# Kernel optimization log

Hardware: AMD Instinct MI355X
Metric: run time of the kernel (lower is better)

The kernel has to match this reference:

```python
import jax, jax.numpy as jnp
import numpy as np

NUM_GRAPHS = 128

def _gcn_conv(x, W, b, src, dst, deg_inv_sqrt, n_nodes):
    # PyG GCNConv: h = X W; out[dst] += d^-1/2[src] * d^-1/2[dst] * h[src]; out += b
    h = x @ W
    norm = deg_inv_sqrt[src] * deg_inv_sqrt[dst]  # [E]
    msg = h[src] * norm[:, None]                  # [E, C]
    out = jax.ops.segment_sum(msg, dst, num_segments=n_nodes)
    return out + b


def setup_inputs() -> dict:
    key = jax.random.key(0)
    k1, k2, k3, k4, k5 = jax.random.split(key, 5)
    n_nodes, n_edges, c_in, c_hid = 50000, 800000, 256, 256
    x = jax.random.normal(k1, (n_nodes, c_in), dtype=jnp.float32)
    edge_index = jax.random.randint(k2, (2, n_edges), 0, n_nodes, dtype=jnp.int64)
    batch = jnp.sort(jax.random.randint(k3, (n_nodes,), 0, NUM_GRAPHS, dtype=jnp.int64))
    s1 = 1.0 / np.sqrt(c_in)
    s2 = 1.0 / np.sqrt(c_hid)
    W1 = jax.random.uniform(k4, (c_in, c_hid), jnp.float32, -s1, s1)
    b1 = jnp.zeros((c_hid,), jnp.float32)
    W2 = jax.random.uniform(k5, (c_hid, c_hid), jnp.float32, -s2, s2)
    b2 = jnp.zeros((c_hid,), jnp.float32)
    return {"x": x, "edge_index": edge_index, "batch": batch,
            "W1": W1, "b1": b1, "W2": W2, "b2": b2}


def reference(x, edge_index, batch, W1, b1, W2, b2):
    n_nodes = x.shape[0]
    # add self-loops (GCNConv default add_self_loops=True)
    loops = jnp.arange(n_nodes, dtype=edge_index.dtype)
    src = jnp.concatenate([edge_index[0], loops])
    dst = jnp.concatenate([edge_index[1], loops])
    deg = jax.ops.segment_sum(jnp.ones_like(dst, dtype=x.dtype), dst, num_segments=n_nodes)
    deg_inv_sqrt = jnp.where(deg > 0, jax.lax.rsqrt(deg), 0.0)

    h = jax.nn.relu(_gcn_conv(x, W1, b1, src, dst, deg_inv_sqrt, n_nodes))
    # dropout p=0.2 is identity in eval mode
    h = jax.nn.relu(_gcn_conv(h, W2, b2, src, dst, deg_inv_sqrt, n_nodes))

    # global mean pool over graph ids
    sums = jax.ops.segment_sum(h, batch, num_segments=NUM_GRAPHS)
    cnts = jax.ops.segment_sum(jnp.ones((n_nodes,), h.dtype), batch, num_segments=NUM_GRAPHS)
    return sums / jnp.maximum(cnts, 1.0)[:, None]
```

## Files before the change

kernel.cpp:

```cpp
#include <hip/hip_runtime.h>

#define NCH 256
#define NS  16

typedef short short8 __attribute__((ext_vector_type(8)));
typedef float f32x4  __attribute__((ext_vector_type(4)));

__device__ __forceinline__ float b2f(unsigned short u) {
    union { unsigned int i; float f; } x; x.i = ((unsigned int)u) << 16; return x.f;
}
__device__ __forceinline__ unsigned short f2b(float f) {
    unsigned int u = __float_as_uint(f);
    unsigned int r = (u + 0x7FFFu + ((u >> 16) & 1u)) >> 16;
    return (unsigned short)r;
}

#define GLOAD_LDS16(gptr, lptr) \
    __builtin_amdgcn_global_load_lds((const __attribute__((address_space(1))) void*)(gptr), \
                                     (__attribute__((address_space(3))) void*)(lptr), 16, 0, 0)

__global__ __launch_bounds__(256) void k_init_deg(int* __restrict__ deg, int n) {
    int i = blockIdx.x * 256 + threadIdx.x;
    if (i < n) deg[i] = 1;
}

__global__ __launch_bounds__(256) void k_hist(const int* __restrict__ dst, int E,
                                              int* __restrict__ deg) {
    int e = blockIdx.x * 256 + threadIdx.x;
    if (e < E) atomicAdd(&deg[dst[e]], 1);
}

__global__ __launch_bounds__(256) void k_scan_blk(const int* __restrict__ deg,
                                                  int* __restrict__ part,
                                                  int* __restrict__ bsum, int N) {
    __shared__ int sm[256];
    int t = threadIdx.x;
    int base = blockIdx.x * 1024 + t * 4;
    int v[4]; int s = 0;
#pragma unroll
    for (int j = 0; j < 4; ++j) {
        int i = base + j;
        int d = (i < N) ? (deg[i] - 1) : 0;
        v[j] = d; s += d;
    }
    sm[t] = s; __syncthreads();
#pragma unroll
    for (int off = 1; off < 256; off <<= 1) {
        int u = (t >= off) ? sm[t - off] : 0;
        __syncthreads();
        sm[t] += u;
        __syncthreads();
    }
    int excl = sm[t] - s;
#pragma unroll
    for (int j = 0; j < 4; ++j) {
        int i = base + j;
        if (i < N) part[i] = excl;
        excl += v[j];
    }
    if (t == 255) bsum[blockIdx.x] = sm[255];
}

__global__ void k_scan_top(int* __restrict__ bsum, int nb, int* __restrict__ rowptr_end) {
    int t = threadIdx.x;
    int orig = (t < nb) ? bsum[t] : 0;
    int v = orig;
#pragma unroll
    for (int off = 1; off < 64; off <<= 1) {
        int u = __shfl_up(v, off, 64);
        if (t >= off) v += u;
    }
    if (t < nb) bsum[t] = v - orig;
    if (t == 63) *rowptr_end = v;
}

__global__ __launch_bounds__(256) void k_finalize(const int* __restrict__ deg,
                                                  int* __restrict__ row_ptr,
                                                  const int* __restrict__ boff,
                                                  int* __restrict__ cursor,
                                                  float* __restrict__ dinv, int N) {
    int i = blockIdx.x * 256 + threadIdx.x;
    if (i < N) {
        int rp = row_ptr[i] + boff[i >> 10];
        row_ptr[i] = rp;
        cursor[i]  = rp;
        dinv[i] = rsqrtf((float)deg[i]);
    }
}

__global__ __launch_bounds__(256) void k_scatter(const int* __restrict__ src,
                                                 const int* __restrict__ dst, int E,
                                                 int* __restrict__ cursor,
                                                 int* __restrict__ col) {
    int e = blockIdx.x * 256 + threadIdx.x;
    if (e < E) {
        int d = dst[e];
        int pos = atomicAdd(&cursor[d], 1);
        col[pos] = src[e];
    }
}

__global__ __launch_bounds__(256) void k_cast8(const float* __restrict__ in,
                                               unsigned short* __restrict__ out, int n8) {
    int i = blockIdx.x * 256 + threadIdx.x;
    if (i < n8) {
        const float4* p = (const float4*)(in + (size_t)i * 8);
        float4 a = p[0], b = p[1];
        unsigned short us[8];
        us[0] = f2b(a.x); us[1] = f2b(a.y); us[2] = f2b(a.z); us[3] = f2b(a.w);
        us[4] = f2b(b.x); us[5] = f2b(b.y); us[6] = f2b(b.z); us[7] = f2b(b.w);
        *(int4*)(out + (size_t)i * 8) = *(const int4*)us;
    }
}

__global__ __launch_bounds__(256) void k_castT(const float* __restrict__ W1,
                                               const float* __restrict__ W2,
                                               unsigned short* __restrict__ Wt1,
                                               unsigned short* __restrict__ Wt2) {
    int k = blockIdx.x, n = threadIdx.x;
    const float* W = blockIdx.y ? W2 : W1;
    unsigned short* Wt = blockIdx.y ? Wt2 : Wt1;
    Wt[(size_t)n * 256 + k] = f2b(W[(size_t)k * 256 + n]);
}

__global__ __launch_bounds__(256) void k_gemm_bf16(const unsigned short* __restrict__ A,
                                                   const unsigned short* __restrict__ Bt,
                                                   unsigned short* __restrict__ C, int M) {
    __shared__ unsigned short As[128 * 32];
    __shared__ unsigned short Bs[128 * 32];

    const int tid  = threadIdx.x;
    const int wid  = tid >> 6;
    const int lane = tid & 63;
    const int m0 = blockIdx.x * 128;
    const int n0 = blockIdx.y * 128;
    const int wr = wid >> 1, wc = wid & 1;

    const int srow = tid >> 2;
    const int skc  = (((tid & 3) ^ (srow & 3)) << 3);
    int arow0 = m0 + srow;       if (arow0 >= M) arow0 = M - 1;
    int arow1 = m0 + srow + 64;  if (arow1 >= M) arow1 = M - 1;
    const int brow0 = n0 + srow;
    const int brow1 = n0 + srow + 64;

    const unsigned short* gA0 = A  + (size_t)arow0 * NCH + skc;
    const unsigned short* gA1 = A  + (size_t)arow1 * NCH + skc;
    const unsigned short* gB0 = Bt + (size_t)brow0 * NCH + skc;
    const unsigned short* gB1 = Bt + (size_t)brow1 * NCH + skc;

    unsigned short* ldsA0 = As + (wid << 9);
    unsigned short* ldsA1 = As + 2048 + (wid << 9);
    unsigned short* ldsB0 = Bs + (wid << 9);
    unsigned short* ldsB1 = Bs + 2048 + (wid << 9);

    f32x4 acc[4][4];
#pragma unroll
    for (int i = 0; i < 4; ++i)
#pragma unroll
        for (int j = 0; j < 4; ++j) acc[i][j] = (f32x4){0.f, 0.f, 0.f, 0.f};

    const int lr = lane & 15;
    const int kcu = lane >> 4;

    for (int k0 = 0; k0 < 256; k0 += 32) {
        __syncthreads();
        GLOAD_LDS16(gA0 + k0, ldsA0);
        GLOAD_LDS16(gA1 + k0, ldsA1);
        GLOAD_LDS16(gB0 + k0, ldsB0);
        GLOAD_LDS16(gB1 + k0, ldsB1);
        __syncthreads();

        short8 af[4], bfr[4];
#pragma unroll
        for (int mf = 0; mf < 4; ++mf) {
            int row = wr * 64 + mf * 16 + lr;
            int lk = ((kcu ^ (row & 3)) << 3);
            af[mf] = *(const short8*)&As[row * 32 + lk];
        }
#pragma unroll
        for (int nf = 0; nf < 4; ++nf) {
            int row = wc * 64 + nf * 16 + lr;
            int lk = ((kcu ^ (row & 3)) << 3);
            bfr[nf] = *(const short8*)&Bs[row * 32 + lk];
        }
#pragma unroll
        for (int mf = 0; mf < 4; ++mf)
#pragma unroll
            for (int nf = 0; nf < 4; ++nf)
                acc[mf][nf] = __builtin_amdgcn_mfma_f32_16x16x32_bf16(af[mf], bfr[nf],
                                                                      acc[mf][nf], 0, 0, 0);
    }

#pragma unroll
    for (int mf = 0; mf < 4; ++mf) {
#pragma unroll
        for (int nf = 0; nf < 4; ++nf) {
            int rb = m0 + wr * 64 + mf * 16 + ((lane >> 4) << 2);
            int cc = n0 + wc * 64 + nf * 16 + lr;
#pragma unroll
            for (int r = 0; r < 4; ++r) {
                int row = rb + r;
                if (row < M) C[(size_t)row * NCH + cc] = f2b(acc[mf][nf][r]);
            }
        }
    }
}

__global__ __launch_bounds__(256) void k_agg_w(const unsigned short* __restrict__ h,
                                               const float* __restrict__ dinv,
                                               const int* __restrict__ row_ptr,
                                               const int* __restrict__ col,
                                               const float* __restrict__ bias,
                                               unsigned short* __restrict__ out, int M) {
    int v = blockIdx.x * 4 + (threadIdx.x >> 6);
    if (v >= M) return;
    const int lane = threadIdx.x & 63;
    const int half = lane >> 5;
    const int cb   = (lane & 31) << 3;

    float acc[8] = {};
    float dv = dinv[v];

    if (half == 0) {
        short8 hv = *(const short8*)&h[(size_t)v * NCH + cb];
#pragma unroll
        for (int i = 0; i < 8; ++i) acc[i] += dv * b2f((unsigned short)hv[i]);
    }

    int beg = row_ptr[v], end = row_ptr[v + 1];
    for (int idx = beg + half; idx < end; idx += 2) {
        int s = col[idx];
        float ws = dinv[s];
        short8 hs = *(const short8*)&h[(size_t)s * NCH + cb];
#pragma unroll
        for (int i = 0; i < 8; ++i) acc[i] += ws * b2f((unsigned short)hs[i]);
    }

#pragma unroll
    for (int i = 0; i < 8; ++i) acc[i] += __shfl_xor(acc[i], 32, 64);

    if (half == 0) {
        f32x4 bl = *(const f32x4*)&bias[cb];
        f32x4 bh = *(const f32x4*)&bias[cb + 4];
        unsigned short us[8];
#pragma unroll
        for (int i = 0; i < 8; ++i) {
            float b = (i < 4) ? bl[i] : bh[i - 4];
            us[i] = f2b(fmaxf(dv * acc[i] + b, 0.0f));
        }
        *(int4*)&out[(size_t)v * NCH + cb] = *(const int4*)us;
    }
}

__device__ __forceinline__ int lower_bound_i(const int* a, int n, int key) {
    int lo = 0, hi = n;
    while (lo < hi) {
        int mid = (lo + hi) >> 1;
        if (a[mid] < key) lo = mid + 1; else hi = mid;
    }
    return lo;
}

__global__ __launch_bounds__(64) void k_pool_a(const unsigned short* __restrict__ a,
                                               const int* __restrict__ batch,
                                               float* __restrict__ partial, int N) {
    int g = blockIdx.x, s = blockIdx.y;
    const int lane = threadIdx.x;
    const int half = lane >> 5;
    const int cb   = (lane & 31) << 3;

    int lo = lower_bound_i(batch, N, g);
    int hi = lower_bound_i(batch, N, g + 1);
    int cnt = hi - lo;
    int len = (cnt + NS - 1) / NS;
    int rlo = lo + s * len;
    int rhi = min(rlo + len, hi);

    float acc[8] = {};
    for (int r = rlo + half; r < rhi; r += 2) {
        short8 hv = *(const short8*)&a[(size_t)r * NCH + cb];
#pragma unroll
        for (int i = 0; i < 8; ++i) acc[i] += b2f((unsigned short)hv[i]);
    }
#pragma unroll
    for (int i = 0; i < 8; ++i) acc[i] += __shfl_xor(acc[i], 32, 64);

    if (half == 0) {
        float* p = partial + ((size_t)g * NS + s) * NCH + cb;
        *(f32x4*)p       = (f32x4){acc[0], acc[1], acc[2], acc[3]};
        *(f32x4*)(p + 4) = (f32x4){acc[4], acc[5], acc[6], acc[7]};
    }
}

__global__ __launch_bounds__(256) void k_pool_b(const float* __restrict__ partial,
                                                const int* __restrict__ batch,
                                                float* __restrict__ out, int N) {
    int g = blockIdx.x, ch = threadIdx.x;
    int lo = lower_bound_i(batch, N, g);
    int hi = lower_bound_i(batch, N, g + 1);
    float s = 0.0f;
#pragma unroll
    for (int k = 0; k < NS; ++k)
        s += partial[((size_t)g * NS + k) * NCH + ch];
    out[(size_t)g * NCH + ch] = s / (float)max(hi - lo, 1);
}

extern "C" void kernel_launch(void* const* d_in, const int* in_sizes, int n_in,
                              void* d_out, int out_size, void* d_ws, size_t ws_size,
                              hipStream_t stream) {
    const float* x     = (const float*)d_in[0];
    const int*   ei    = (const int*)d_in[1];
    const int*   batch = (const int*)d_in[2];
    const float* W1    = (const float*)d_in[3];
    const float* b1    = (const float*)d_in[4];
    const float* W2    = (const float*)d_in[5];
    const float* b2    = (const float*)d_in[6];
    float* out = (float*)d_out;

    const int M = in_sizes[0] / NCH;
    const int E = in_sizes[1] / 2;
    const int* src = ei;
    const int* dst = ei + E;

    char* w = (char*)d_ws;
    auto alloc = [&](size_t bytes) -> void* {
        void* p = (void*)w;
        w += (bytes + 255) & ~(size_t)255;
        return p;
    };
    int*   deg     = (int*)alloc((size_t)M * 4);
    float* dinv    = (float*)alloc((size_t)M * 4);
    int*   row_ptr = (int*)alloc((size_t)(M + 1) * 4);
    int*   cursor  = (int*)alloc((size_t)M * 4);
    int*   bsum    = (int*)alloc(64 * 4);
    int*   col     = (int*)alloc((size_t)E * 4);
    unsigned short* xb   = (unsigned short*)alloc((size_t)M * NCH * 2);
    unsigned short* bufP = (unsigned short*)alloc((size_t)M * NCH * 2);
    unsigned short* bufQ = (unsigned short*)alloc((size_t)M * NCH * 2);
    unsigned short* Wt1  = (unsigned short*)alloc((size_t)NCH * NCH * 2);
    unsigned short* Wt2  = (unsigned short*)alloc((size_t)NCH * NCH * 2);
    float* partial = (float*)alloc((size_t)128 * NS * NCH * 4);

    const int nb = (M + 1023) / 1024;

    k_cast8<<<(M * NCH / 8 + 255) / 256, 256, 0, stream>>>(x, xb, M * NCH / 8);
    k_castT<<<dim3(256, 2), 256, 0, stream>>>(W1, W2, Wt1, Wt2);

    k_init_deg<<<(M + 255) / 256, 256, 0, stream>>>(deg, M);
    k_hist<<<(E + 255) / 256, 256, 0, stream>>>(dst, E, deg);
    k_scan_blk<<<nb, 256, 0, stream>>>(deg, row_ptr, bsum, M);
    k_scan_top<<<1, 64, 0, stream>>>(bsum, nb, row_ptr + M);
    k_finalize<<<(M + 255) / 256, 256, 0, stream>>>(deg, row_ptr, bsum, cursor, dinv, M);
    k_scatter<<<(E + 255) / 256, 256, 0, stream>>>(src, dst, E, cursor, col);

    dim3 ggrid((M + 127) / 128, NCH / 128);

    k_gemm_bf16<<<ggrid, 256, 0, stream>>>(xb, Wt1, bufP, M);
    k_agg_w<<<(M + 3) / 4, 256, 0, stream>>>(bufP, dinv, row_ptr, col, b1, bufQ, M);
    k_gemm_bf16<<<ggrid, 256, 0, stream>>>(bufQ, Wt2, bufP, M);
    k_agg_w<<<(M + 3) / 4, 256, 0, stream>>>(bufP, dinv, row_ptr, col, b2, bufQ, M);
    k_pool_a<<<dim3(128, NS), 64, 0, stream>>>(bufQ, batch, partial, M);
    k_pool_b<<<128, 256, 0, stream>>>(partial, batch, out, M);
}
```

Measured before the change: 303.3 us.

## Use register-resident weight GEMM and prefetch packed edge weights in aggregation

Replaces the LDS-tiled GEMM with a persistent kernel in which each wave keeps its 64-column slice of the bf16 weight matrix in registers. Each block streams 16-row A tiles straight from global memory, double-buffering the next tile in registers. A new pre-pass packs each edge's source index and dinv[src] into an int2 array, so aggregation does one load per edge instead of two dependent ones. The aggregation loop is software-pipelined to keep two edges per half-wave in flight. The costs are high register pressure in the GEMM, no LDS sharing of A, an extra E-sized buffer, and one more kernel launch.

```diff
diff --git a/kernel.cpp b/kernel.cpp
--- a/kernel.cpp
+++ b/kernel.cpp
@@ -14,10 +14,6 @@
     unsigned int r = (u + 0x7FFFu + ((u >> 16) & 1u)) >> 16;
     return (unsigned short)r;
 }
-
-#define GLOAD_LDS16(gptr, lptr) \
-    __builtin_amdgcn_global_load_lds((const __attribute__((address_space(1))) void*)(gptr), \
-                                     (__attribute__((address_space(3))) void*)(lptr), 16, 0, 0)
 
 __global__ __launch_bounds__(256) void k_init_deg(int* __restrict__ deg, int n) {
     int i = blockIdx.x * 256 + threadIdx.x;
@@ -100,6 +96,16 @@
     }
 }
 
+__global__ __launch_bounds__(256) void k_wprep(const int* __restrict__ col,
+                                               const float* __restrict__ dinv,
+                                               int2* __restrict__ cw, int E) {
+    int i = blockIdx.x * 256 + threadIdx.x;
+    if (i < E) {
+        int s = col[i];
+        cw[i] = make_int2(s, __float_as_int(dinv[s]));
+    }
+}
+
 __global__ __launch_bounds__(256) void k_cast8(const float* __restrict__ in,
                                                unsigned short* __restrict__ out, int n8) {
     int i = blockIdx.x * 256 + threadIdx.x;
@@ -123,93 +129,73 @@
     Wt[(size_t)n * 256 + k] = f2b(W[(size_t)k * 256 + n]);
 }
 
-__global__ __launch_bounds__(256) void k_gemm_bf16(const unsigned short* __restrict__ A,
-                                                   const unsigned short* __restrict__ Bt,
-                                                   unsigned short* __restrict__ C, int M) {
-    __shared__ unsigned short As[128 * 32];
-    __shared__ unsigned short Bs[128 * 32];
-
+__device__ __forceinline__ void a_load(const unsigned short* __restrict__ A,
+                                       int tile, int M, int lr, int ku, short8* dst) {
+    int row = tile * 16 + lr; if (row >= M) row = M - 1;
+    const unsigned short* pa = A + (size_t)row * NCH + ku * 8;
+#pragma unroll
+    for (int ks = 0; ks < 8; ++ks) dst[ks] = *(const short8*)(pa + ks * 32);
+}
+
+__global__ __launch_bounds__(256, 2) void k_gemm_rs(const unsigned short* __restrict__ A,
+                                                    const unsigned short* __restrict__ Bt,
+                                                    unsigned short* __restrict__ C, int M) {
     const int tid  = threadIdx.x;
     const int wid  = tid >> 6;
     const int lane = tid & 63;
-    const int m0 = blockIdx.x * 128;
-    const int n0 = blockIdx.y * 128;
-    const int wr = wid >> 1, wc = wid & 1;
-
-    const int srow = tid >> 2;
-    const int skc  = (((tid & 3) ^ (srow & 3)) << 3);
-    int arow0 = m0 + srow;       if (arow0 >= M) arow0 = M - 1;
-    int arow1 = m0 + srow + 64;  if (arow1 >= M) arow1 = M - 1;
-    const int brow0 = n0 + srow;
-    const int brow1 = n0 + srow + 64;
-
-    const unsigned short* gA0 = A  + (size_t)arow0 * NCH + skc;
-    const unsigned short* gA1 = A  + (size_t)arow1 * NCH + skc;
-    const unsigned short* gB0 = Bt + (size_t)brow0 * NCH + skc;
-    const unsigned short* gB1 = Bt + (size_t)brow1 * NCH + skc;
-
-    unsigned short* ldsA0 = As + (wid << 9);
-    unsigned short* ldsA1 = As + 2048 + (wid << 9);
-    unsigned short* ldsB0 = Bs + (wid << 9);
-    unsigned short* ldsB1 = Bs + 2048 + (wid << 9);
-
-    f32x4 acc[4][4];
-#pragma unroll
-    for (int i = 0; i < 4; ++i)
-#pragma unroll
-        for (int j = 0; j < 4; ++j) acc[i][j] = (f32x4){0.f, 0.f, 0.f, 0.f};
-
-    const int lr = lane & 15;
-    const int kcu = lane >> 4;
-
-    for (int k0 = 0; k0 < 256; k0 += 32) {
-        __syncthreads();
-        GLOAD_LDS16(gA0 + k0, ldsA0);
-        GLOAD_LDS16(gA1 + k0, ldsA1);
-        GLOAD_LDS16(gB0 + k0, ldsB0);
-        GLOAD_LDS16(gB1 + k0, ldsB1);
-        __syncthreads();
-
-        short8 af[4], bfr[4];
-#pragma unroll
-        for (int mf = 0; mf < 4; ++mf) {
-            int row = wr * 64 + mf * 16 + lr;
-            int lk = ((kcu ^ (row & 3)) << 3);
-            af[mf] = *(const short8*)&As[row * 32 + lk];
-        }
+    const int lr   = lane & 15;
+    const int ku   = lane >> 4;
+
+    short8 bfr[4][8];
+    {
+        const unsigned short* pb = Bt + (size_t)(wid * 64 + lr) * NCH + ku * 8;
+#pragma unroll
+        for (int nf = 0; nf < 4; ++nf)
+#pragma unroll
+            for (int ks = 0; ks < 8; ++ks)
+                bfr[nf][ks] = *(const short8*)(pb + nf * 16 * NCH + ks * 32);
+    }
+
+    const int tiles = (M + 15) >> 4;
+    int t = blockIdx.x;
+
+    short8 afA[8], afB[8];
+    if (t < tiles) a_load(A, t, M, lr, ku, afA);
+
+    for (; t < tiles; t += gridDim.x) {
+        int tn = t + gridDim.x;
+        if (tn < tiles) a_load(A, tn, M, lr, ku, afB);
+
+        f32x4 acc[4];
+#pragma unroll
+        for (int nf = 0; nf < 4; ++nf) acc[nf] = (f32x4){0.f, 0.f, 0.f, 0.f};
+
+#pragma unroll
+        for (int ks = 0; ks < 8; ++ks)
+#pragma unroll
+            for (int nf = 0; nf < 4; ++nf)
+                acc[nf] = __builtin_amdgcn_mfma_f32_16x16x32_bf16(afA[ks], bfr[nf][ks],
+                                                                  acc[nf], 0, 0, 0);
+
+        int rb = t * 16 + ku * 4;
 #pragma unroll
         for (int nf = 0; nf < 4; ++nf) {
-            int row = wc * 64 + nf * 16 + lr;
-            int lk = ((kcu ^ (row & 3)) << 3);
-            bfr[nf] = *(const short8*)&Bs[row * 32 + lk];
-        }
-#pragma unroll
-        for (int mf = 0; mf < 4; ++mf)
-#pragma unroll
-            for (int nf = 0; nf < 4; ++nf)
-                acc[mf][nf] = __builtin_amdgcn_mfma_f32_16x16x32_bf16(af[mf], bfr[nf],
-                                                                      acc[mf][nf], 0, 0, 0);
-    }
-
-#pragma unroll
-    for (int mf = 0; mf < 4; ++mf) {
-#pragma unroll
-        for (int nf = 0; nf < 4; ++nf) {
-            int rb = m0 + wr * 64 + mf * 16 + ((lane >> 4) << 2);
-            int cc = n0 + wc * 64 + nf * 16 + lr;
+            int col = wid * 64 + nf * 16 + lr;
 #pragma unroll
             for (int r = 0; r < 4; ++r) {
                 int row = rb + r;
-                if (row < M) C[(size_t)row * NCH + cc] = f2b(acc[mf][nf][r]);
+                if (row < M) C[(size_t)row * NCH + col] = f2b(acc[nf][r]);
             }
         }
+#pragma unroll
+        for (int ks = 0; ks < 8; ++ks) afA[ks] = afB[ks];
     }
 }
 
 __global__ __launch_bounds__(256) void k_agg_w(const unsigned short* __restrict__ h,
                                                const float* __restrict__ dinv,
                                                const int* __restrict__ row_ptr,
-                                               const int* __restrict__ col,
+                                               const int2* __restrict__ cw,
                                                const float* __restrict__ bias,
                                                unsigned short* __restrict__ out, int M) {
     int v = blockIdx.x * 4 + (threadIdx.x >> 6);
@@ -221,19 +207,51 @@
     float acc[8] = {};
     float dv = dinv[v];
 
+    int beg = row_ptr[v], end = row_ptr[v + 1];
+    int i0 = beg + half * 2;
+
+    short8 rs = {};
+    if (half == 0) rs = *(const short8*)&h[(size_t)v * NCH + cb];
+
+    short8 r0 = {}, r1 = {};
+    float  w0 = 0.f, w1 = 0.f;
+    bool b0 = i0 < end, b1 = i0 + 1 < end;
+    if (b0) {
+        int2 e = cw[i0];
+        r0 = *(const short8*)&h[(size_t)e.x * NCH + cb];
+        w0 = __int_as_float(e.y);
+    }
+    if (b1) {
+        int2 e = cw[i0 + 1];
+        r1 = *(const short8*)&h[(size_t)e.x * NCH + cb];
+        w1 = __int_as_float(e.y);
+    }
+
+    while (b0) {
+        int in = i0 + 4;
+        bool n0 = in < end, n1 = in + 1 < end;
+        short8 s0 = {}, s1 = {};
+        float  x0 = 0.f, x1 = 0.f;
+        if (n0) {
+            int2 e = cw[in];
+            s0 = *(const short8*)&h[(size_t)e.x * NCH + cb];
+            x0 = __int_as_float(e.y);
+        }
+        if (n1) {
+            int2 e = cw[in + 1];
+            s1 = *(const short8*)&h[(size_t)e.x * NCH + cb];
+            x1 = __int_as_float(e.y);
+        }
+#pragma unroll
+        for (int i = 0; i < 8; ++i) acc[i] += w0 * b2f((unsigned short)r0[i]);
+#pragma unroll
+        for (int i = 0; i < 8; ++i) acc[i] += w1 * b2f((unsigned short)r1[i]);
+        r0 = s0; r1 = s1; w0 = x0; w1 = x1; b0 = n0; b1 = n1; i0 = in;
+    }
+
     if (half == 0) {
-        short8 hv = *(const short8*)&h[(size_t)v * NCH + cb];
-#pragma unroll
-        for (int i = 0; i < 8; ++i) acc[i] += dv * b2f((unsigned short)hv[i]);
-    }
-
-    int beg = row_ptr[v], end = row_ptr[v + 1];
-    for (int idx = beg + half; idx < end; idx += 2) {
-        int s = col[idx];
-        float ws = dinv[s];
-        short8 hs = *(const short8*)&h[(size_t)s * NCH + cb];
-#pragma unroll
-        for (int i = 0; i < 8; ++i) acc[i] += ws * b2f((unsigned short)hs[i]);
+#pragma unroll
+        for (int i = 0; i < 8; ++i) acc[i] += dv * b2f((unsigned short)rs[i]);
     }
 
 #pragma unroll
@@ -334,6 +352,7 @@
     int*   cursor  = (int*)alloc((size_t)M * 4);
     int*   bsum    = (int*)alloc(64 * 4);
     int*   col     = (int*)alloc((size_t)E * 4);
+    int2*  cw      = (int2*)alloc((size_t)E * 8);
     unsigned short* xb   = (unsigned short*)alloc((size_t)M * NCH * 2);
     unsigned short* bufP = (unsigned short*)alloc((size_t)M * NCH * 2);
     unsigned short* bufQ = (unsigned short*)alloc((size_t)M * NCH * 2);
@@ -352,13 +371,14 @@
     k_scan_top<<<1, 64, 0, stream>>>(bsum, nb, row_ptr + M);
     k_finalize<<<(M + 255) / 256, 256, 0, stream>>>(deg, row_ptr, bsum, cursor, dinv, M);
     k_scatter<<<(E + 255) / 256, 256, 0, stream>>>(src, dst, E, cursor, col);
-
-    dim3 ggrid((M + 127) / 128, NCH / 128);
-
-    k_gemm_bf16<<<ggrid, 256, 0, stream>>>(xb, Wt1, bufP, M);
-    k_agg_w<<<(M + 3) / 4, 256, 0, stream>>>(bufP, dinv, row_ptr, col, b1, bufQ, M);
-    k_gemm_bf16<<<ggrid, 256, 0, stream>>>(bufQ, Wt2, bufP, M);
-    k_agg_w<<<(M + 3) / 4, 256, 0, stream>>>(bufP, dinv, row_ptr, col, b2, bufQ, M);
+    k_wprep<<<(E + 255) / 256, 256, 0, stream>>>(col, dinv, cw, E);
+
+    const int ggrid = 512;
+
+    k_gemm_rs<<<ggrid, 256, 0, stream>>>(xb, Wt1, bufP, M);
+    k_agg_w<<<(M + 3) / 4, 256, 0, stream>>>(bufP, dinv, row_ptr, cw, b1, bufQ, M);
+    k_gemm_rs<<<ggrid, 256, 0, stream>>>(bufQ, Wt2, bufP, M);
+    k_agg_w<<<(M + 3) / 4, 256, 0, stream>>>(bufP, dinv, row_ptr, cw, b2, bufQ, M);
     k_pool_a<<<dim3(128, NS), 64, 0, stream>>>(bufQ, batch, partial, M);
     k_pool_b<<<128, 256, 0, stream>>>(partial, batch, out, M);
 }
```

Result: slower. 314.1 us (+3.5%).
